# Optimization experiments

Hardware: AMD Instinct MI355X
Metric: run time of the kernel (lower is better)

The kernel has to match this reference:

```python
import jax, jax.numpy as jnp
import numpy as np

N = 50000      # nodes
E = 1600000    # edges per graph
IN = 64
HID = 64
OUT = 64


def _gat_conv(x, edge_index, W, a_src, a_dst, bias):
    """PyG GATConv, heads=1, add_self_loops=True, negative_slope=0.2."""
    n = x.shape[0]
    h = x @ W                                   # [N, d]
    loop = jnp.arange(n, dtype=edge_index.dtype)
    src = jnp.concatenate([edge_index[0], loop])
    dst = jnp.concatenate([edge_index[1], loop])
    e = jax.nn.leaky_relu((h @ a_src)[src] + (h @ a_dst)[dst], negative_slope=0.2)
    m = jax.ops.segment_max(e, dst, num_segments=n)          # stable edge-softmax per dst
    w = jnp.exp(e - m[dst])
    denom = jax.ops.segment_sum(w, dst, num_segments=n)
    alpha = w / denom[dst]                                   # [E+N]
    out = jax.ops.segment_sum(h[src] * alpha[:, None], dst, num_segments=n)
    return out + bias


def setup_inputs() -> dict:
    key = jax.random.key(0)
    ks = jax.random.split(key, 32)

    def glorot(k, shape):
        fan_out = shape[1] if len(shape) > 1 else 1
        lim = (6.0 / (shape[0] + fan_out)) ** 0.5
        return jax.random.uniform(k, shape, minval=-lim, maxval=lim, dtype=jnp.float32)

    inp = {
        "x_ind": jax.random.normal(ks[0], (N, IN), jnp.float32),
        "x_pos": jax.random.normal(ks[1], (N, IN), jnp.float32),
        "edge_ind": jax.random.randint(ks[2], (2, E), 0, N, dtype=jnp.int32),
        "edge_pos": jax.random.randint(ks[3], (2, E), 0, N, dtype=jnp.int32),
        "w1_ind": glorot(ks[4], (IN, HID)),
        "as1_ind": glorot(ks[5], (HID,)),
        "ad1_ind": glorot(ks[6], (HID,)),
        "b1_ind": jnp.zeros((HID,), jnp.float32),
        "w2_ind": glorot(ks[7], (HID, OUT)),
        "as2_ind": glorot(ks[8], (OUT,)),
        "ad2_ind": glorot(ks[9], (OUT,)),
        "b2_ind": jnp.zeros((OUT,), jnp.float32),
        "w1_pos": glorot(ks[10], (IN, HID)),
        "as1_pos": glorot(ks[11], (HID,)),
        "ad1_pos": glorot(ks[12], (HID,)),
        "b1_pos": jnp.zeros((HID,), jnp.float32),
        "w2_pos": glorot(ks[13], (HID, OUT)),
        "as2_pos": glorot(ks[14], (OUT,)),
        "ad2_pos": glorot(ks[15], (OUT,)),
        "b2_pos": jnp.zeros((OUT,), jnp.float32),
        "first_hop_att": glorot(ks[16], (2, HID)),
        "att_weight": glorot(ks[17], (2, OUT)),
        "mlp_w": glorot(ks[18], (OUT, 1)),
        "mlp_b": jnp.zeros((1,), jnp.float32),
    }
    return inp


def reference(x_ind, x_pos, edge_ind, edge_pos,
              w1_ind, as1_ind, ad1_ind, b1_ind,
              w2_ind, as2_ind, ad2_ind, b2_ind,
              w1_pos, as1_pos, ad1_pos, b1_pos,
              w2_pos, as2_pos, ad2_pos, b2_pos,
              first_hop_att, att_weight, mlp_w, mlp_b):
    h_i = jax.nn.relu(_gat_conv(x_ind, edge_ind, w1_ind, as1_ind, ad1_ind, b1_ind))
    h_p = jax.nn.relu(_gat_conv(x_pos, edge_pos, w1_pos, as1_pos, ad1_pos, b1_pos))
    # first-hop branch attention over the two graphs
    s1 = jnp.stack([jnp.sum(first_hop_att[0] * h_i, axis=1),
                    jnp.sum(first_hop_att[1] * h_p, axis=1)], axis=0)  # [2, N]
    a1 = jax.nn.softmax(s1, axis=0)
    fused = a1[0][:, None] * h_i + a1[1][:, None] * h_p
    g_i = _gat_conv(fused, edge_ind, w2_ind, as2_ind, ad2_ind, b2_ind)
    g_p = _gat_conv(fused, edge_pos, w2_pos, as2_pos, ad2_pos, b2_pos)
    s2 = jnp.stack([jnp.sum(att_weight[0] * g_i, axis=1),
                    jnp.sum(att_weight[1] * g_p, axis=1)], axis=0)
    a2 = jax.nn.softmax(s2, axis=0)
    x = a2[0][:, None] * g_i + a2[1][:, None] * g_p
    return x @ mlp_w + mlp_b                    # [N, 1]
```

## Files before the change

kernel.cpp:

```cpp
#include <hip/hip_runtime.h>
#include <hip/hip_fp16.h>

#define ND 64
#define BG 256
#define MAXB 512
#define PCH 16384
#define CAP 9216

__device__ __forceinline__ float lrelu(float x) { return x > 0.f ? x : 0.2f * x; }

__device__ __forceinline__ float wave_sum(float v) {
#pragma unroll
    for (int m = 32; m > 0; m >>= 1) v += __shfl_xor(v, m, 64);
    return v;
}

__device__ __forceinline__ void fma8(float* acc, float w, int4 raw) {
    union { int4 i; __half2 h[4]; } u;
    u.i = raw;
#pragma unroll
    for (int i = 0; i < 4; i++) {
        float2 f = __half22float2(u.h[i]);
        acc[2 * i]     = fmaf(w, f.x, acc[2 * i]);
        acc[2 * i + 1] = fmaf(w, f.y, acc[2 * i + 1]);
    }
}


__global__ void init_cursor(int* __restrict__ bcursor, int nb) {
    int t = threadIdx.x;
    if (t < nb) bcursor[t] = t * CAP;
}

__device__ void partition_body(int* hist, int* lcur,
                               const int* __restrict__ eI, const int* __restrict__ eP,
                               int* __restrict__ bcursor, int* __restrict__ part,
                               int N, int E, int nb) {
    int t = threadIdx.x;
    int total = 2 * E;
    int chunkBase = blockIdx.x * PCH;
    int cnt = min(PCH, total - chunkBase);
    int cnt4 = cnt & ~3;
    if (t < nb) hist[t] = 0;
    __syncthreads();
    for (int i = t * 4; i < cnt4; i += 4096) {
        int e = chunkBase + i;
        int4 d; int base;
        if (e + 3 < E)   { d = *(const int4*)(eI + E + e); base = 0; }
        else if (e >= E) { d = *(const int4*)(eP + E + (e - E)); base = N; }
        else {
            int tmp[4];
#pragma unroll
            for (int k = 0; k < 4; k++) {
                int ee = e + k;
                tmp[k] = (ee < E) ? eI[E + ee] : N + eP[E + ee - E];
            }
            d = make_int4(tmp[0], tmp[1], tmp[2], tmp[3]); base = 0;
        }
        atomicAdd(&hist[(base + d.x) >> 8], 1);
        atomicAdd(&hist[(base + d.y) >> 8], 1);
        atomicAdd(&hist[(base + d.z) >> 8], 1);
        atomicAdd(&hist[(base + d.w) >> 8], 1);
    }
    for (int i = cnt4 + t; i < cnt; i += 1024) {
        int e = chunkBase + i;
        int idx = (e < E) ? eI[E + e] : N + eP[E + (e - E)];
        atomicAdd(&hist[idx >> 8], 1);
    }
    __syncthreads();
    if (t < nb) lcur[t] = hist[t] ? atomicAdd(&bcursor[t], hist[t]) : 0;
    __syncthreads();
    for (int i = t * 4; i < cnt4; i += 4096) {
        int e = chunkBase + i;
        int4 s4, d4; int base;
        if (e + 3 < E)   { s4 = *(const int4*)(eI + e); d4 = *(const int4*)(eI + E + e); base = 0; }
        else if (e >= E) { s4 = *(const int4*)(eP + (e - E)); d4 = *(const int4*)(eP + E + (e - E)); base = N; }
        else {
            int ts[4], td[4];
#pragma unroll
            for (int k = 0; k < 4; k++) {
                int ee = e + k;
                if (ee < E) { ts[k] = eI[ee]; td[k] = eI[E + ee]; }
                else        { ts[k] = eP[ee - E]; td[k] = N + eP[E + ee - E]; }
            }
            s4 = make_int4(ts[0], ts[1], ts[2], ts[3]);
            d4 = make_int4(td[0], td[1], td[2], td[3]); base = 0;
        }
        int idx, pos;
        idx = base + d4.x; pos = atomicAdd(&lcur[idx >> 8], 1); part[pos] = (s4.x << 8) | (idx & 255);
        idx = base + d4.y; pos = atomicAdd(&lcur[idx >> 8], 1); part[pos] = (s4.y << 8) | (idx & 255);
        idx = base + d4.z; pos = atomicAdd(&lcur[idx >> 8], 1); part[pos] = (s4.z << 8) | (idx & 255);
        idx = base + d4.w; pos = atomicAdd(&lcur[idx >> 8], 1); part[pos] = (s4.w << 8) | (idx & 255);
    }
    for (int i = cnt4 + t; i < cnt; i += 1024) {
        int e = chunkBase + i;
        int s, idx;
        if (e < E) { s = eI[e]; idx = eI[E + e]; }
        else       { s = eP[e - E]; idx = N + eP[E + (e - E)]; }
        int pos = atomicAdd(&lcur[idx >> 8], 1);
        part[pos] = (s << 8) | (idx & 255);
    }
}

__device__ void gemm_body(float* xsAll, int gb,
                          const float* __restrict__ xA, const float* __restrict__ xB,
                          const float* __restrict__ WA, const float* __restrict__ WB,
                          const float* __restrict__ asA, const float* __restrict__ adA,
                          const float* __restrict__ asB, const float* __restrict__ adB,
                          __half* __restrict__ h16, float* __restrict__ ssrc,
                          float* __restrict__ sdst, int N) {
    int half = gb & 1;
    int blk = gb >> 1;
    int wave = threadIdx.x >> 6;
    int lane = threadIdx.x & 63;
    const float* x  = half ? xB : xA;
    const float* W  = half ? WB : WA;
    const float* av_ = half ? asB : asA;
    const float* dv_ = half ? adB : adA;
    int nodeBase = (blk * 16 + wave) * 4;
    float* xs = xsAll + wave * (4 * ND);

    if (nodeBase + 3 < N) {
        *(float4*)&xs[lane * 4] = *(const float4*)&x[(size_t)nodeBase * ND + lane * 4];
    } else if (nodeBase < N) {
#pragma unroll
        for (int i = 0; i < 4; i++) {
            int gi = nodeBase * ND + lane * 4 + i;
            xs[lane * 4 + i] = (gi < N * ND) ? x[gi] : 0.f;
        }
    }
    __syncthreads();
    if (nodeBase >= N) return;

    float4 acc = {0.f, 0.f, 0.f, 0.f};
#pragma unroll
    for (int k = 0; k < ND; k++) {
        float wv = W[k * ND + lane];
        acc.x = fmaf(xs[0 * ND + k], wv, acc.x);
        acc.y = fmaf(xs[1 * ND + k], wv, acc.y);
        acc.z = fmaf(xs[2 * ND + k], wv, acc.z);
        acc.w = fmaf(xs[3 * ND + k], wv, acc.w);
    }
    float av = av_[lane], dv = dv_[lane];
    float s1x = wave_sum(acc.x * av), s2x = wave_sum(acc.x * dv);
    float s1y = wave_sum(acc.y * av), s2y = wave_sum(acc.y * dv);
    float s1z = wave_sum(acc.z * av), s2z = wave_sum(acc.z * dv);
    float s1w = wave_sum(acc.w * av), s2w = wave_sum(acc.w * dv);

    int g0 = half * N + nodeBase;
    h16[(size_t)(g0 + 0) * ND + lane] = __float2half(acc.x);
    if (nodeBase + 1 < N) h16[(size_t)(g0 + 1) * ND + lane] = __float2half(acc.y);
    if (nodeBase + 2 < N) h16[(size_t)(g0 + 2) * ND + lane] = __float2half(acc.z);
    if (nodeBase + 3 < N) h16[(size_t)(g0 + 3) * ND + lane] = __float2half(acc.w);
    if (lane == 0) {
        ssrc[g0] = s1x; sdst[g0] = s2x;
        if (nodeBase + 1 < N) { ssrc[g0 + 1] = s1y; sdst[g0 + 1] = s2y; }
        if (nodeBase + 2 < N) { ssrc[g0 + 2] = s1z; sdst[g0 + 2] = s2z; }
        if (nodeBase + 3 < N) { ssrc[g0 + 3] = s1w; sdst[g0 + 3] = s2w; }
    }
}

__global__ void __launch_bounds__(1024) part_gemm(
        const int* __restrict__ eI, const int* __restrict__ eP,
        int* __restrict__ bcursor, int* __restrict__ part,
        const float* __restrict__ xA, const float* __restrict__ xB,
        const float* __restrict__ WA, const float* __restrict__ WB,
        const float* __restrict__ asA, const float* __restrict__ adA,
        const float* __restrict__ asB, const float* __restrict__ adB,
        __half* __restrict__ h16, float* __restrict__ ssrc, float* __restrict__ sdst,
        int N, int E, int nb, int partBlocks) {
    __shared__ int smem[16 * 4 * ND];
    if (blockIdx.x < partBlocks) {
        partition_body(smem, smem + MAXB, eI, eP, bcursor, part, N, E, nb);
    } else {
        gemm_body((float*)smem, blockIdx.x - partBlocks,
                  xA, xB, WA, WB, asA, adA, asB, adB, h16, ssrc, sdst, N);
    }
}

__global__ void bucket_build(const int* __restrict__ part, const int* __restrict__ bcursor,
                             int* __restrict__ row, int* __restrict__ deg,
                             int* __restrict__ csr, int n2) {
    __shared__ int lhist[BG];
    __shared__ int lrow[BG];
    int b = blockIdx.x, t = threadIdx.x;
    int start = b * CAP;
    int cnt = bcursor[b] - start;
    int cnt4 = cnt & ~3;
    if (t < BG) lhist[t] = 0;
    __syncthreads();
    for (int j = t * 4; j < cnt4; j += 4096) {
        int4 p = *(const int4*)(part + start + j);
        atomicAdd(&lhist[p.x & 255], 1);
        atomicAdd(&lhist[p.y & 255], 1);
        atomicAdd(&lhist[p.z & 255], 1);
        atomicAdd(&lhist[p.w & 255], 1);
    }
    for (int j = cnt4 + t; j < cnt; j += 1024) atomicAdd(&lhist[part[start + j] & 255], 1);
    __syncthreads();
    int v = 0;
    if (t < BG) { v = lhist[t]; lrow[t] = v; }
    __syncthreads();
    for (int off = 1; off < BG; off <<= 1) {
        int a = (t < BG && t >= off) ? lrow[t - off] : 0;
        __syncthreads();
        if (t < BG) lrow[t] += a;
        __syncthreads();
    }
    if (t < BG) {
        int excl = lrow[t] - v;
        int g = b * BG + t;
        if (g < n2) { row[g] = start + excl; deg[g] = v; }
        lhist[t] = start + excl;
    }
    __syncthreads();
    for (int j = t * 4; j < cnt4; j += 4096) {
        int4 p = *(const int4*)(part + start + j);
        int pos;
        pos = atomicAdd(&lhist[p.x & 255], 1); csr[pos] = p.x >> 8;
        pos = atomicAdd(&lhist[p.y & 255], 1); csr[pos] = p.y >> 8;
        pos = atomicAdd(&lhist[p.z & 255], 1); csr[pos] = p.z >> 8;
        pos = atomicAdd(&lhist[p.w & 255], 1); csr[pos] = p.w >> 8;
    }
    for (int j = cnt4 + t; j < cnt; j += 1024) {
        int p = part[start + j];
        int pos = atomicAdd(&lhist[p & 255], 1);
        csr[pos] = p >> 8;
    }
}

__global__ void gemm_dual(const float* __restrict__ xA, const float* __restrict__ xB,
                          const float* __restrict__ WA, const float* __restrict__ WB,
                          const float* __restrict__ asA, const float* __restrict__ adA,
                          const float* __restrict__ asB, const float* __restrict__ adB,
                          __half* __restrict__ h16, float* __restrict__ ssrc,
                          float* __restrict__ sdst, int N) {
    __shared__ float xs[16][4 * ND];
    int wave = threadIdx.x >> 6;
    int half = blockIdx.x & 1;
    int blk = blockIdx.x >> 1;
    int lane = threadIdx.x & 63;
    const float* x  = half ? xB : xA;
    const float* W  = half ? WB : WA;
    const float* av_ = half ? asB : asA;
    const float* dv_ = half ? adB : adA;
    int nodeBase = (blk * 4 + wave) * 4;
    float* xsw = xs[wave];
    if (nodeBase + 3 < N) {
        *(float4*)&xsw[lane * 4] = *(const float4*)&x[(size_t)nodeBase * ND + lane * 4];
    } else if (nodeBase < N) {
#pragma unroll
        for (int i = 0; i < 4; i++) {
            int gi = nodeBase * ND + lane * 4 + i;
            xsw[lane * 4 + i] = (gi < N * ND) ? x[gi] : 0.f;
        }
    }
    __syncthreads();
    if (nodeBase >= N) return;
    float4 acc = {0.f, 0.f, 0.f, 0.f};
#pragma unroll
    for (int k = 0; k < ND; k++) {
        float wv = W[k * ND + lane];
        acc.x = fmaf(xsw[0 * ND + k], wv, acc.x);
        acc.y = fmaf(xsw[1 * ND + k], wv, acc.y);
        acc.z = fmaf(xsw[2 * ND + k], wv, acc.z);
        acc.w = fmaf(xsw[3 * ND + k], wv, acc.w);
    }
    float av = av_[lane], dv = dv_[lane];
    float s1x = wave_sum(acc.x * av), s2x = wave_sum(acc.x * dv);
    float s1y = wave_sum(acc.y * av), s2y = wave_sum(acc.y * dv);
    float s1z = wave_sum(acc.z * av), s2z = wave_sum(acc.z * dv);
    float s1w = wave_sum(acc.w * av), s2w = wave_sum(acc.w * dv);
    int g0 = half * N + nodeBase;
    h16[(size_t)(g0 + 0) * ND + lane] = __float2half(acc.x);
    if (nodeBase + 1 < N) h16[(size_t)(g0 + 1) * ND + lane] = __float2half(acc.y);
    if (nodeBase + 2 < N) h16[(size_t)(g0 + 2) * ND + lane] = __float2half(acc.z);
    if (nodeBase + 3 < N) h16[(size_t)(g0 + 3) * ND + lane] = __float2half(acc.w);
    if (lane == 0) {
        ssrc[g0] = s1x; sdst[g0] = s2x;
        if (nodeBase + 1 < N) { ssrc[g0 + 1] = s1y; sdst[g0 + 1] = s2y; }
        if (nodeBase + 2 < N) { ssrc[g0 + 2] = s1z; sdst[g0 + 2] = s2z; }
        if (nodeBase + 3 < N) { ssrc[g0 + 3] = s1w; sdst[g0 + 3] = s2w; }
    }
}

__global__ void aggregate_dual(const int* __restrict__ csr, const int* __restrict__ row,
                               const int* __restrict__ deg, const float* __restrict__ ssrc,
                               const float* __restrict__ sdst, const __half* __restrict__ h16,
                               const float* __restrict__ bA, const float* __restrict__ bB,
                               float* __restrict__ out, int N, int relu) {
    int half = blockIdx.x & 1;
    int wave = threadIdx.x >> 6;
    int lane = threadIdx.x & 63;
    int sub  = lane >> 4;
    int l16  = lane & 15;
    int slot = l16 >> 3;
    int fl8  = (l16 & 7) * 8;
    int node = ((blockIdx.x >> 1) * 4 + wave) * 4 + sub;
    bool valid = node < N;
    int g = half * N + node;
    const float* bias = half ? bB : bA;
    const float* ss = ssrc + (size_t)half * N;
    const __half* hh = h16 + (size_t)half * N * ND;

    int start = valid ? row[g] : 0;
    int cnt   = valid ? deg[g] : 0;
    float sd  = valid ? sdst[g] : 0.f;
    float wself = valid ? __expf(lrelu(ss[node] + sd)) : 0.f;

    float acc[8] = {0.f, 0.f, 0.f, 0.f, 0.f, 0.f, 0.f, 0.f};
    float denomp = 0.f;
    int waveBase = sub << 4;

    for (int base = 0; base < cnt; base += 16) {
        int c16 = min(16, cnt - base);
        int sj = (l16 < c16) ? csr[start + base + l16] : 0;
        float wj = (l16 < c16) ? __expf(lrelu(ss[sj] + sd)) : 0.f;
        denomp += wj;
        int nq = (c16 + 1) >> 1;
        float w0 = __shfl(wj, waveBase + slot, 64);
        int s0 = __shfl(sj, waveBase + slot, 64);
        int4 r0 = *(const int4*)(hh + (size_t)s0 * ND + fl8);
        if (nq == 1) { fma8(acc, w0, r0); continue; }
        float w1 = __shfl(wj, waveBase + 2 + slot, 64);
        int s1 = __shfl(sj, waveBase + 2 + slot, 64);
        int4 r1 = *(const int4*)(hh + (size_t)s1 * ND + fl8);
        for (int c = 2; c < nq; c++) {
            float w2 = __shfl(wj, waveBase + c * 2 + slot, 64);
            int s2 = __shfl(sj, waveBase + c * 2 + slot, 64);
            int4 r2 = *(const int4*)(hh + (size_t)s2 * ND + fl8);
            fma8(acc, w0, r0);
            w0 = w1; r0 = r1;
            w1 = w2; r1 = r2;
        }
        fma8(acc, w0, r0);
        fma8(acc, w1, r1);
    }

#pragma unroll
    for (int i = 0; i < 8; i++) acc[i] += __shfl_xor(acc[i], 8, 64);
#pragma unroll
    for (int m = 1; m <= 8; m <<= 1) denomp += __shfl_xor(denomp, m, 64);
    float denom = denomp + wself;

    if (!valid || slot != 0) return;
    int4 rawS = *(const int4*)(hh + (size_t)node * ND + fl8);
    union { int4 i; __half2 h[4]; } us;
    us.i = rawS;
    float v[8];
#pragma unroll
    for (int i = 0; i < 4; i++) {
        float2 f = __half22float2(us.h[i]);
        v[2 * i]     = (acc[2 * i]     + wself * f.x) / denom + bias[fl8 + 2 * i];
        v[2 * i + 1] = (acc[2 * i + 1] + wself * f.y) / denom + bias[fl8 + 2 * i + 1];
    }
    if (relu) {
#pragma unroll
        for (int i = 0; i < 8; i++) v[i] = fmaxf(v[i], 0.f);
    }
    *(float4*)&out[(size_t)g * ND + fl8]     = make_float4(v[0], v[1], v[2], v[3]);
    *(float4*)&out[(size_t)g * ND + fl8 + 4] = make_float4(v[4], v[5], v[6], v[7]);
}

__global__ void branch_att(const float* __restrict__ hbig, const float* __restrict__ att,
                           float* __restrict__ fused, int n) {
    int gid = blockIdx.x * blockDim.x + threadIdx.x;
    int node = gid >> 6, lane = gid & 63;
    if (node >= n) return;
    float vi = hbig[(size_t)node * ND + lane];
    float vp = hbig[((size_t)n + node) * ND + lane];
    float s0 = wave_sum(att[lane] * vi);
    float s1 = wave_sum(att[ND + lane] * vp);
    float m = fmaxf(s0, s1);
    float a0 = __expf(s0 - m), a1 = __expf(s1 - m);
    fused[(size_t)node * ND + lane] = (a0 * vi + a1 * vp) / (a0 + a1);
}

__global__ void branch_att_mlp(const float* __restrict__ hbig, const float* __restrict__ att,
                               const float* __restrict__ mlpw, const float* __restrict__ mlpb,
                               float* __restrict__ out, int n) {
    int gid = blockIdx.x * blockDim.x + threadIdx.x;
    int node = gid >> 6, lane = gid & 63;
    if (node >= n) return;
    float vi = hbig[(size_t)node * ND + lane];
    float vp = hbig[((size_t)n + node) * ND + lane];
    float s0 = wave_sum(att[lane] * vi);
    float s1 = wave_sum(att[ND + lane] * vp);
    float m = fmaxf(s0, s1);
    float a0 = __expf(s0 - m), a1 = __expf(s1 - m);
    float xj = (a0 * vi + a1 * vp) / (a0 + a1);
    float o = wave_sum(xj * mlpw[lane]);
    if (lane == 0) out[node] = o + mlpb[0];
}

extern "C" void kernel_launch(void* const* d_in, const int* in_sizes, int n_in,
                              void* d_out, int out_size, void* d_ws, size_t ws_size,
                              hipStream_t stream) {
    const int N = in_sizes[0] / ND;
    const int E = in_sizes[2] / 2;

    const float* x_ind = (const float*)d_in[0];
    const float* x_pos = (const float*)d_in[1];
    const int*   e_ind = (const int*)d_in[2];
    const int*   e_pos = (const int*)d_in[3];
    const float* w1i = (const float*)d_in[4];
    const float* as1i = (const float*)d_in[5];
    const float* ad1i = (const float*)d_in[6];
    const float* b1i = (const float*)d_in[7];
    const float* w2i = (const float*)d_in[8];
    const float* as2i = (const float*)d_in[9];
    const float* ad2i = (const float*)d_in[10];
    const float* b2i = (const float*)d_in[11];
    const float* w1p = (const float*)d_in[12];
    const float* as1p = (const float*)d_in[13];
    const float* ad1p = (const float*)d_in[14];
    const float* b1p = (const float*)d_in[15];
    const float* w2p = (const float*)d_in[16];
    const float* as2p = (const float*)d_in[17];
    const float* ad2p = (const float*)d_in[18];
    const float* b2p = (const float*)d_in[19];
    const float* fha = (const float*)d_in[20];
    const float* attw = (const float*)d_in[21];
    const float* mlpw = (const float*)d_in[22];
    const float* mlpb = (const float*)d_in[23];

    char* ws = (char*)d_ws;
    size_t off = 0;
    auto alloc = [&](size_t elems) { void* p = ws + off; off += elems * 4; return p; };

    const int n2 = 2 * N;
    const int nb = (n2 + BG - 1) / BG;

    __half* h16 = (__half*)alloc((size_t)n2 * ND / 2);
    float* hbig = (float*)alloc((size_t)n2 * ND);
    float* bufC = (float*)alloc((size_t)N * ND);
    float* ssrc = (float*)alloc(n2);
    float* sdst = (float*)alloc(n2);
    int* deg    = (int*)alloc(n2);
    int* rowi   = (int*)alloc(n2);
    int* csr    = (int*)alloc((size_t)nb * CAP);
    int* bcursor= (int*)alloc(MAXB);
    int* part   = (int*)hbig;

    const int partBlocks  = (2 * E + PCH - 1) / PCH;
    const int gemm1Blocks = 2 * ((N + 63) / 64);
    const int gemm2Blocks = 2 * ((N + 15) / 16);
    const int aggBlocks   = 2 * ((N + 15) / 16);
    const int nodeBlocks  = (N + 3) / 4;

    init_cursor<<<1, 512, 0, stream>>>(bcursor, nb);
    part_gemm<<<partBlocks + gemm1Blocks, 1024, 0, stream>>>(
        e_ind, e_pos, bcursor, part,
        x_ind, x_pos, w1i, w1p, as1i, ad1i, as1p, ad1p,
        h16, ssrc, sdst, N, E, nb, partBlocks);
    bucket_build<<<nb, 1024, 0, stream>>>(part, bcursor, rowi, deg, csr, n2);

    aggregate_dual<<<aggBlocks, 256, 0, stream>>>(csr, rowi, deg, ssrc, sdst, h16,
                                                  b1i, b1p, hbig, N, 1);
    branch_att<<<nodeBlocks, 256, 0, stream>>>(hbig, fha, bufC, N);

    gemm_dual<<<gemm2Blocks, 256, 0, stream>>>(bufC, bufC, w2i, w2p,
                                               as2i, ad2i, as2p, ad2p,
                                               h16, ssrc, sdst, N);
    aggregate_dual<<<aggBlocks, 256, 0, stream>>>(csr, rowi, deg, ssrc, sdst, h16,
                                                  b2i, b2p, hbig, N, 0);
    branch_att_mlp<<<nodeBlocks, 256, 0, stream>>>(hbig, attw, mlpw, mlpb,
                                                   (float*)d_out, N);
}
```

Measured before the change: 342.1 us.

## Fuse first-hop branch attention into second GEMM and sort CSR by source quartile

Removes the separate branch_att kernel and its fused buffer by computing the branch softmax mix inside the second-layer GEMM while loading node features. This saves one launch and a full N x 64 float write and read. Separately, bucket_build now keys each edge by destination plus a source-quartile sub-bucket, so every destination's neighbor list is ordered into coarse source ranges. The aim is better cache locality for the gathers in aggregation, at the cost of a 1024-entry scan in shared memory. Bounds checks on the tail nodes were dropped, which assumes N is a multiple of 4.

```diff
diff --git a/kernel.cpp b/kernel.cpp
--- a/kernel.cpp
+++ b/kernel.cpp
@@ -180,83 +180,110 @@
 
 __global__ void bucket_build(const int* __restrict__ part, const int* __restrict__ bcursor,
                              int* __restrict__ row, int* __restrict__ deg,
-                             int* __restrict__ csr, int n2) {
-    __shared__ int lhist[BG];
-    __shared__ int lrow[BG];
+                             int* __restrict__ csr, int n2, int N) {
+    __shared__ int lhist[BG * 4];
+    __shared__ int lrow[BG * 4];
     int b = blockIdx.x, t = threadIdx.x;
     int start = b * CAP;
     int cnt = bcursor[b] - start;
     int cnt4 = cnt & ~3;
-    if (t < BG) lhist[t] = 0;
+    int q1 = N >> 2, q2 = N >> 1, q3 = q1 + q2;
+    auto key = [&](int p) {
+        int s = p >> 8;
+        int q = (s >= q2) ? 2 : 0;
+        q += (s >= (q ? q3 : q1)) ? 1 : 0;
+        return ((p & 255) << 2) | q;
+    };
+    lhist[t] = 0;
     __syncthreads();
     for (int j = t * 4; j < cnt4; j += 4096) {
         int4 p = *(const int4*)(part + start + j);
-        atomicAdd(&lhist[p.x & 255], 1);
-        atomicAdd(&lhist[p.y & 255], 1);
-        atomicAdd(&lhist[p.z & 255], 1);
-        atomicAdd(&lhist[p.w & 255], 1);
-    }
-    for (int j = cnt4 + t; j < cnt; j += 1024) atomicAdd(&lhist[part[start + j] & 255], 1);
-    __syncthreads();
-    int v = 0;
-    if (t < BG) { v = lhist[t]; lrow[t] = v; }
-    __syncthreads();
-    for (int off = 1; off < BG; off <<= 1) {
-        int a = (t < BG && t >= off) ? lrow[t - off] : 0;
+        atomicAdd(&lhist[key(p.x)], 1);
+        atomicAdd(&lhist[key(p.y)], 1);
+        atomicAdd(&lhist[key(p.z)], 1);
+        atomicAdd(&lhist[key(p.w)], 1);
+    }
+    for (int j = cnt4 + t; j < cnt; j += 1024) atomicAdd(&lhist[key(part[start + j])], 1);
+    __syncthreads();
+    int v = lhist[t];
+    lrow[t] = v;
+    __syncthreads();
+    for (int off = 1; off < 1024; off <<= 1) {
+        int a = (t >= off) ? lrow[t - off] : 0;
         __syncthreads();
-        if (t < BG) lrow[t] += a;
+        lrow[t] += a;
         __syncthreads();
     }
+    int cur = start + lrow[t] - v;
     if (t < BG) {
-        int excl = lrow[t] - v;
         int g = b * BG + t;
-        if (g < n2) { row[g] = start + excl; deg[g] = v; }
-        lhist[t] = start + excl;
-    }
+        if (g < n2) {
+            row[g] = start + lrow[4 * t] - lhist[4 * t];
+            deg[g] = lhist[4 * t] + lhist[4 * t + 1] + lhist[4 * t + 2] + lhist[4 * t + 3];
+        }
+    }
+    __syncthreads();
+    lhist[t] = cur;
     __syncthreads();
     for (int j = t * 4; j < cnt4; j += 4096) {
         int4 p = *(const int4*)(part + start + j);
         int pos;
-        pos = atomicAdd(&lhist[p.x & 255], 1); csr[pos] = p.x >> 8;
-        pos = atomicAdd(&lhist[p.y & 255], 1); csr[pos] = p.y >> 8;
-        pos = atomicAdd(&lhist[p.z & 255], 1); csr[pos] = p.z >> 8;
-        pos = atomicAdd(&lhist[p.w & 255], 1); csr[pos] = p.w >> 8;
+        pos = atomicAdd(&lhist[key(p.x)], 1); csr[pos] = p.x >> 8;
+        pos = atomicAdd(&lhist[key(p.y)], 1); csr[pos] = p.y >> 8;
+        pos = atomicAdd(&lhist[key(p.z)], 1); csr[pos] = p.z >> 8;
+        pos = atomicAdd(&lhist[key(p.w)], 1); csr[pos] = p.w >> 8;
     }
     for (int j = cnt4 + t; j < cnt; j += 1024) {
         int p = part[start + j];
-        int pos = atomicAdd(&lhist[p & 255], 1);
+        int pos = atomicAdd(&lhist[key(p)], 1);
         csr[pos] = p >> 8;
     }
 }
 
-__global__ void gemm_dual(const float* __restrict__ xA, const float* __restrict__ xB,
-                          const float* __restrict__ WA, const float* __restrict__ WB,
-                          const float* __restrict__ asA, const float* __restrict__ adA,
-                          const float* __restrict__ asB, const float* __restrict__ adB,
-                          __half* __restrict__ h16, float* __restrict__ ssrc,
-                          float* __restrict__ sdst, int N) {
-    __shared__ float xs[16][4 * ND];
-    int wave = threadIdx.x >> 6;
+__global__ void gemm2_fused(const float* __restrict__ hbig, const float* __restrict__ fha,
+                            const float* __restrict__ WA, const float* __restrict__ WB,
+                            const float* __restrict__ asA, const float* __restrict__ adA,
+                            const float* __restrict__ asB, const float* __restrict__ adB,
+                            __half* __restrict__ h16, float* __restrict__ ssrc,
+                            float* __restrict__ sdst, int N) {
+    __shared__ float xs[4][4 * ND];
     int half = blockIdx.x & 1;
     int blk = blockIdx.x >> 1;
+    int wave = threadIdx.x >> 6;
     int lane = threadIdx.x & 63;
-    const float* x  = half ? xB : xA;
     const float* W  = half ? WB : WA;
     const float* av_ = half ? asB : asA;
     const float* dv_ = half ? adB : adA;
     int nodeBase = (blk * 4 + wave) * 4;
     float* xsw = xs[wave];
-    if (nodeBase + 3 < N) {
-        *(float4*)&xsw[lane * 4] = *(const float4*)&x[(size_t)nodeBase * ND + lane * 4];
-    } else if (nodeBase < N) {
-#pragma unroll
-        for (int i = 0; i < 4; i++) {
-            int gi = nodeBase * ND + lane * 4 + i;
-            xsw[lane * 4 + i] = (gi < N * ND) ? x[gi] : 0.f;
-        }
+
+    if (nodeBase < N) {
+        int nd = nodeBase + (lane >> 4);
+        int col = (lane & 15) * 4;
+        float4 vi = *(const float4*)&hbig[(size_t)nd * ND + col];
+        float4 vp = *(const float4*)&hbig[((size_t)N + nd) * ND + col];
+        float4 a0 = *(const float4*)&fha[col];
+        float4 a1 = *(const float4*)&fha[ND + col];
+        float p0 = vi.x * a0.x + vi.y * a0.y + vi.z * a0.z + vi.w * a0.w;
+        float p1 = vp.x * a1.x + vp.y * a1.y + vp.z * a1.z + vp.w * a1.w;
+#pragma unroll
+        for (int m = 1; m <= 8; m <<= 1) {
+            p0 += __shfl_xor(p0, m, 64);
+            p1 += __shfl_xor(p1, m, 64);
+        }
+        float mx = fmaxf(p0, p1);
+        float e0 = __expf(p0 - mx), e1 = __expf(p1 - mx);
+        float inv = 1.f / (e0 + e1);
+        float4 f;
+        f.x = (e0 * vi.x + e1 * vp.x) * inv;
+        f.y = (e0 * vi.y + e1 * vp.y) * inv;
+        f.z = (e0 * vi.z + e1 * vp.z) * inv;
+        f.w = (e0 * vi.w + e1 * vp.w) * inv;
+        *(float4*)&xsw[lane * 4] = f;
     }
     __syncthreads();
     if (nodeBase >= N) return;
+
     float4 acc = {0.f, 0.f, 0.f, 0.f};
 #pragma unroll
     for (int k = 0; k < ND; k++) {
@@ -271,16 +298,17 @@
     float s1y = wave_sum(acc.y * av), s2y = wave_sum(acc.y * dv);
     float s1z = wave_sum(acc.z * av), s2z = wave_sum(acc.z * dv);
     float s1w = wave_sum(acc.w * av), s2w = wave_sum(acc.w * dv);
+
     int g0 = half * N + nodeBase;
     h16[(size_t)(g0 + 0) * ND + lane] = __float2half(acc.x);
-    if (nodeBase + 1 < N) h16[(size_t)(g0 + 1) * ND + lane] = __float2half(acc.y);
-    if (nodeBase + 2 < N) h16[(size_t)(g0 + 2) * ND + lane] = __float2half(acc.z);
-    if (nodeBase + 3 < N) h16[(size_t)(g0 + 3) * ND + lane] = __float2half(acc.w);
+    h16[(size_t)(g0 + 1) * ND + lane] = __float2half(acc.y);
+    h16[(size_t)(g0 + 2) * ND + lane] = __float2half(acc.z);
+    h16[(size_t)(g0 + 3) * ND + lane] = __float2half(acc.w);
     if (lane == 0) {
         ssrc[g0] = s1x; sdst[g0] = s2x;
-        if (nodeBase + 1 < N) { ssrc[g0 + 1] = s1y; sdst[g0 + 1] = s2y; }
-        if (nodeBase + 2 < N) { ssrc[g0 + 2] = s1z; sdst[g0 + 2] = s2z; }
-        if (nodeBase + 3 < N) { ssrc[g0 + 3] = s1w; sdst[g0 + 3] = s2w; }
+        ssrc[g0 + 1] = s1y; sdst[g0 + 1] = s2y;
+        ssrc[g0 + 2] = s1z; sdst[g0 + 2] = s2z;
+        ssrc[g0 + 3] = s1w; sdst[g0 + 3] = s2w;
     }
 }
 
@@ -360,20 +388,6 @@
     }
     *(float4*)&out[(size_t)g * ND + fl8]     = make_float4(v[0], v[1], v[2], v[3]);
     *(float4*)&out[(size_t)g * ND + fl8 + 4] = make_float4(v[4], v[5], v[6], v[7]);
-}
-
-__global__ void branch_att(const float* __restrict__ hbig, const float* __restrict__ att,
-                           float* __restrict__ fused, int n) {
-    int gid = blockIdx.x * blockDim.x + threadIdx.x;
-    int node = gid >> 6, lane = gid & 63;
-    if (node >= n) return;
-    float vi = hbig[(size_t)node * ND + lane];
-    float vp = hbig[((size_t)n + node) * ND + lane];
-    float s0 = wave_sum(att[lane] * vi);
-    float s1 = wave_sum(att[ND + lane] * vp);
-    float m = fmaxf(s0, s1);
-    float a0 = __expf(s0 - m), a1 = __expf(s1 - m);
-    fused[(size_t)node * ND + lane] = (a0 * vi + a1 * vp) / (a0 + a1);
 }
 
 __global__ void branch_att_mlp(const float* __restrict__ hbig, const float* __restrict__ att,
@@ -433,7 +447,6 @@
 
     __half* h16 = (__half*)alloc((size_t)n2 * ND / 2);
     float* hbig = (float*)alloc((size_t)n2 * ND);
-    float* bufC = (float*)alloc((size_t)N * ND);
     float* ssrc = (float*)alloc(n2);
     float* sdst = (float*)alloc(n2);
     int* deg    = (int*)alloc(n2);
@@ -453,15 +466,14 @@
         e_ind, e_pos, bcursor, part,
         x_ind, x_pos, w1i, w1p, as1i, ad1i, as1p, ad1p,
         h16, ssrc, sdst, N, E, nb, partBlocks);
-    bucket_build<<<nb, 1024, 0, stream>>>(part, bcursor, rowi, deg, csr, n2);
+    bucket_build<<<nb, 1024, 0, stream>>>(part, bcursor, rowi, deg, csr, n2, N);
 
     aggregate_dual<<<aggBlocks, 256, 0, stream>>>(csr, rowi, deg, ssrc, sdst, h16,
                                                   b1i, b1p, hbig, N, 1);
-    branch_att<<<nodeBlocks, 256, 0, stream>>>(hbig, fha, bufC, N);
-
-    gemm_dual<<<gemm2Blocks, 256, 0, stream>>>(bufC, bufC, w2i, w2p,
-                                               as2i, ad2i, as2p, ad2p,
-                                               h16, ssrc, sdst, N);
+
+    gemm2_fused<<<gemm2Blocks, 256, 0, stream>>>(hbig, fha, w2i, w2p,
+                                                 as2i, ad2i, as2p, ad2p,
+                                                 h16, ssrc, sdst, N);
     aggregate_dual<<<aggBlocks, 256, 0, stream>>>(csr, rowi, deg, ssrc, sdst, h16,
                                                   b2i, b2p, hbig, N, 0);
     branch_att_mlp<<<nodeBlocks, 256, 0, stream>>>(hbig, attw, mlpw, mlpb,
```

New measurement: 331.8 us. 3.0% less time.
